# Performance work log

Measured on AMD Instinct MI355X. Metric: run time of the kernel, lower is better.

## Reference

```python
import jax, jax.numpy as jnp
import numpy as np

NUM = 8          # nlk*nlk - 1
IDX_REF = 4      # center neighbor index


def _gather2d(img, yi, xi):
    # img: (B,H,W); yi,xi: int32 (B,K,H,W) already clipped in-range
    B, H, W = img.shape
    flat = img.reshape(B, H * W)
    idx = (yi * W + xi).reshape(B, -1)
    return jnp.take_along_axis(flat, idx, axis=1).reshape(yi.shape)


def _bilinear(img, ys, xs):
    # bilinear sample with zero padding outside (deform-conv v2 semantics)
    # img: (B,H,W); ys,xs: float (B,K,H,W)
    B, H, W = img.shape
    y0 = jnp.floor(ys)
    x0 = jnp.floor(xs)
    y0i = y0.astype(jnp.int32)
    x0i = x0.astype(jnp.int32)
    wy1 = ys - y0
    wx1 = xs - x0
    out = jnp.zeros(ys.shape, img.dtype)
    for dy, wy in ((0, 1.0 - wy1), (1, wy1)):
        for dx, wx in ((0, 1.0 - wx1), (1, wx1)):
            yy = y0i + dy
            xx = x0i + dx
            valid = ((yy >= 0) & (yy < H) & (xx >= 0) & (xx < W)).astype(img.dtype)
            v = _gather2d(img, jnp.clip(yy, 0, H - 1), jnp.clip(xx, 0, W - 1))
            out = out + wy * wx * valid * v
    return out


def _conv3(x, w):
    return jax.lax.conv_general_dilated(x, w, (1, 1), ((1, 1), (1, 1)),
                                        dimension_numbers=('NCHW', 'OIHW', 'NCHW'))


def _bn_relu(x, g, b, m, v):
    s = g / jnp.sqrt(v + 1e-5)
    return jax.nn.relu(x * s[None, :, None, None] + (b - m * s)[None, :, None, None])


def _disp_warp(right, disp):
    # sample right image at x' = x - disparity, bilinear along width, zeros outside
    B, C, H, W = right.shape
    xs = jnp.arange(W, dtype=right.dtype)[None, None, :] - disp[:, 0]  # (B,H,W)
    x0 = jnp.floor(xs)
    x0i = x0.astype(jnp.int32)
    w1 = xs - x0
    out = jnp.zeros_like(right)
    for d, w in ((0, 1.0 - w1), (1, w1)):
        xi = x0i + d
        valid = ((xi >= 0) & (xi < W)).astype(right.dtype)
        v = jnp.take_along_axis(right, jnp.clip(xi, 0, W - 1)[:, None], axis=3)
        out = out + (w * valid)[:, None] * v
    return out


def _forward(coarse_disparity, normal_estimation, left_image, right_image, confidence,
             conv1_w, bn1_g, bn1_b, bn1_m, bn1_v,
             conv2_w, bn2_g, bn2_b, bn2_m, bn2_v,
             conv3_w, aff_scale_const):
    B, _, H, W = coarse_disparity.shape
    # current_scale == 1 => interpolate is identity, disp_ == coarse_disparity
    warped_error = _disp_warp(right_image, coarse_disparity) - left_image
    guidance = jnp.concatenate([normal_estimation, left_image, right_image, warped_error], axis=1)

    x = _bn_relu(_conv3(guidance, conv1_w), bn1_g, bn1_b, bn1_m, bn1_v)
    x = _bn_relu(_conv3(x, conv2_w), bn2_g, bn2_b, bn2_m, bn2_v)
    oa = _conv3(x, conv3_w)                                   # (B, 3*NUM, H, W)

    o1, o2, aff = oa[:, :NUM], oa[:, NUM:2 * NUM], oa[:, 2 * NUM:]
    # torch: cat((o1,o2),1).view(B,NUM,2,H,W) -> faithful pairing of channels
    off = jnp.concatenate([o1, o2], axis=1).reshape(B, NUM, 2, H, W)
    zero_c = jnp.zeros((B, 1, 2, H, W), off.dtype)
    off9 = jnp.concatenate([off[:, :IDX_REF], zero_c, off[:, IDX_REF:]], axis=1)  # (B,9,2,H,W)

    aff = jnp.tanh(aff) / (aff_scale_const + 1e-8)            # TGASS

    # confidence gather at p + offset_k (1x1 deform conv, w_conf=1), offsets detached
    ii = jnp.arange(H, dtype=off.dtype)[None, None, :, None]
    jj = jnp.arange(W, dtype=off.dtype)[None, None, None, :]
    off_nc = jax.lax.stop_gradient(
        jnp.concatenate([off9[:, :IDX_REF], off9[:, IDX_REF + 1:]], axis=1))  # (B,8,2,H,W)
    conf_aff = _bilinear(confidence[:, 0], ii + off_nc[:, :, 0], jj + off_nc[:, :, 1])
    aff = aff * conf_aff

    s = jnp.sum(jnp.abs(aff), axis=1, keepdims=True) + 1e-4
    s = jnp.maximum(s, 1.0)                                   # TGASS clamp
    aff = aff / s
    aff_ref = 1.0 - jnp.sum(aff, axis=1, keepdims=True)
    aff9 = jnp.concatenate([aff[:, :IDX_REF], aff_ref, aff[:, IDX_REF:]], axis=1)  # (B,9,H,W)

    # one propagation: modulated deformable 3x3 conv, all-ones weight, zero bias
    ky = (jnp.arange(9, dtype=off.dtype) // 3 - 1.0)[None, :, None, None]
    kx = (jnp.arange(9, dtype=off.dtype) % 3 - 1.0)[None, :, None, None]
    sampled = _bilinear(coarse_disparity[:, 0], ii + ky + off9[:, :, 0], jj + kx + off9[:, :, 1])
    inter = jnp.sum(aff9 * sampled, axis=1, keepdims=True)    # (B,1,H,W)
    inter = inter * (inter >= 0).astype(inter.dtype)
    inter = jnp.maximum(inter, 0.0)
    final = jnp.maximum(0.7 * coarse_disparity + 0.3 * inter, 0.0)
    return final


def setup_inputs() -> dict:
    key = jax.random.key(0)
    ks = jax.random.split(key, 20)
    B, H, W = 4, 384, 1280
    inp = {}
    inp['coarse_disparity'] = jax.random.uniform(ks[0], (B, 1, H, W), jnp.float32) * 40.0
    inp['normal_estimation'] = jax.random.normal(ks[1], (B, 3, H, W), jnp.float32)
    inp['left_image'] = jax.random.uniform(ks[2], (B, 3, H, W), jnp.float32)
    inp['right_image'] = jax.random.uniform(ks[3], (B, 3, H, W), jnp.float32)
    inp['confidence'] = jax.random.uniform(ks[4], (B, 1, H, W), jnp.float32)
    inp['conv1_w'] = jax.random.normal(ks[5], (32, 12, 3, 3), jnp.float32) * 0.05
    inp['bn1_g'] = jax.random.uniform(ks[6], (32,), jnp.float32) + 0.5
    inp['bn1_b'] = jax.random.normal(ks[7], (32,), jnp.float32) * 0.1
    inp['bn1_m'] = jax.random.normal(ks[8], (32,), jnp.float32) * 0.1
    inp['bn1_v'] = jax.random.uniform(ks[9], (32,), jnp.float32) + 0.5
    inp['conv2_w'] = jax.random.normal(ks[10], (64, 32, 3, 3), jnp.float32) * 0.05
    inp['bn2_g'] = jax.random.uniform(ks[11], (64,), jnp.float32) + 0.5
    inp['bn2_b'] = jax.random.normal(ks[12], (64,), jnp.float32) * 0.1
    inp['bn2_m'] = jax.random.normal(ks[13], (64,), jnp.float32) * 0.1
    inp['bn2_v'] = jax.random.uniform(ks[14], (64,), jnp.float32) + 0.5
    inp['conv3_w'] = jax.random.normal(ks[15], (3 * NUM, 64, 3, 3), jnp.float32) * 0.05
    inp['aff_scale_const'] = jnp.array([1.0 * NUM], jnp.float32)  # affinity_gamma * num
    return inp


def reference(coarse_disparity, normal_estimation, left_image, right_image, confidence,
              conv1_w, bn1_g, bn1_b, bn1_m, bn1_v,
              conv2_w, bn2_g, bn2_b, bn2_m, bn2_v,
              conv3_w, aff_scale_const):
    return _forward(coarse_disparity, normal_estimation, left_image, right_image, confidence,
                    conv1_w, bn1_g, bn1_b, bn1_m, bn1_v,
                    conv2_w, bn2_g, bn2_b, bn2_m, bn2_v,
                    conv3_w, aff_scale_const)
```

## Files before the change

kernel.cpp:

```cpp
#include <hip/hip_runtime.h>
#include <math.h>

static constexpr int B_ = 4;
static constexpr int H_ = 384;
static constexpr int W_ = 1280;
static constexpr int HW_ = H_ * W_;

typedef _Float16 f16x8 __attribute__((ext_vector_type(8)));
typedef float f32x4 __attribute__((ext_vector_type(4)));


template <int C_IN, int C_OUT>
__global__ __launch_bounds__(256) void prep_w(const float* __restrict__ w,
                                              unsigned short* __restrict__ wb)
{
  constexpr int CICH = C_IN / 32;
  constexpr int NCOT = (C_OUT + 15) / 16;
  constexpr int NE = NCOT * CICH * 9 * 512;
  int i = blockIdx.x * 256 + threadIdx.x;
  if (i >= NE) return;
  int k   = i & 31;
  int row = (i >> 5) & 15;
  int ts  = i >> 9;
  int s   = ts % 9;
  int tc  = ts / 9;
  int c   = tc % CICH;
  int t   = tc / CICH;
  int co  = t * 16 + row;
  int ci  = c * 32 + k;
  float v = 0.f;
  if (co < C_OUT) v = w[((size_t)co * C_IN + ci) * 9 + s];
  union { _Float16 f; unsigned short u; } ch;
  ch.f = (_Float16)v;
  wb[i] = ch.u;
}

__global__ __launch_bounds__(256) void prep_w1(const float* __restrict__ w,
                                               unsigned short* __restrict__ wb)
{
  constexpr int NE = 2 * 6 * 512;
  int i = blockIdx.x * 256 + threadIdx.x;
  if (i >= NE) return;
  int k    = i & 31;
  int row  = (i >> 5) & 15;
  int ts   = i >> 9;
  int chunk = ts % 6;
  int tc   = ts / 6;
  int ky   = chunk >> 1;
  int kc   = chunk & 1;
  int kx, ci;
  bool valid;
  if (kc == 0) { kx = k >> 4;  ci = k & 15; valid = (ci < 12); }
  else         { kx = 2;       ci = k & 15; valid = (k < 16) && (ci < 12); }
  int co = tc * 16 + row;
  float v = valid ? w[((size_t)co * 12 + ci) * 9 + ky * 3 + kx] : 0.f;
  union { _Float16 f; unsigned short u; } ch;
  ch.f = (_Float16)v;
  wb[i] = ch.u;
}

__global__ __launch_bounds__(256, 4) void conv1_mfma(
    const float* __restrict__ disp, const float* __restrict__ normal,
    const float* __restrict__ left, const float* __restrict__ right,
    const unsigned short* __restrict__ wb,
    const float* __restrict__ bn_g, const float* __restrict__ bn_b,
    const float* __restrict__ bn_m, const float* __restrict__ bn_v,
    unsigned short* __restrict__ out,
    int b0, int out_y0, int out_rows)
{
  constexpr int NCOT = 2;
  constexpr int TY  = 8;
  constexpr int HR  = 10;
  constexpr int TXI = 36;

  __shared__ unsigned short smem[HR * TXI * 16];

  const int tilesX = W_ / 32;
  int bb = blockIdx.x;
  const int txi = bb % tilesX; bb /= tilesX;
  const int tilesY = (out_rows + TY - 1) / TY;
  const int tyi = bb % tilesY;
  const int gi  = bb / tilesY;
  const int b   = b0 + gi;
  const int x0  = txi * 32;
  const int oy0 = out_y0 + tyi * TY;

  const int tid    = threadIdx.x;
  const int w      = tid >> 6;
  const int lane15 = tid & 15;
  const int kgrp   = (tid >> 4) & 3;
  const int aoff   = lane15 * 32 + kgrp * 8;

  f32x4 acc[NCOT][2][2];
#pragma unroll
  for (int i = 0; i < NCOT; i++)
#pragma unroll
    for (int rr = 0; rr < 2; rr++) {
      acc[i][rr][0] = (f32x4){0.f, 0.f, 0.f, 0.f};
      acc[i][rr][1] = (f32x4){0.f, 0.f, 0.f, 0.f};
    }

  for (int it = tid; it < HR * TXI; it += 256) {
    int row = it / TXI;
    int px  = it - row * TXI;
    int gy  = oy0 - 1 + row;
    int gx  = x0 - 2 + px;
    union { _Float16 f[16]; uint4 u[2]; } R;
    R.u[0] = (uint4){0, 0, 0, 0};
    R.u[1] = (uint4){0, 0, 0, 0};
    if (((unsigned)gy < (unsigned)H_) & ((unsigned)gx < (unsigned)W_)) {
      size_t p = (size_t)gy * W_ + gx;
      float d = disp[(size_t)b * HW_ + p];
      float xs = (float)gx - d;
      float x0f = floorf(xs);
      int xi0 = (int)x0f;
      float w1 = xs - x0f;
      int xi1 = xi0 + 1;
      float v0 = (xi0 >= 0 && xi0 < W_) ? 1.f : 0.f;
      float v1 = (xi1 >= 0 && xi1 < W_) ? 1.f : 0.f;
      int xc0 = min(max(xi0, 0), W_ - 1);
      int xc1 = min(max(xi1, 0), W_ - 1);
      float w0f = (1.f - w1) * v0;
      float w1f = w1 * v1;
#pragma unroll
      for (int c = 0; c < 3; c++) {
        const float* rrow = right + (size_t)(b * 3 + c) * HW_ + (size_t)gy * W_;
        float l = left[(size_t)(b * 3 + c) * HW_ + p];
        float n = normal[(size_t)(b * 3 + c) * HW_ + p];
        float r = rrow[gx];
        float warped = w0f * rrow[xc0] + w1f * rrow[xc1];
        R.f[c]     = (_Float16)n;
        R.f[3 + c] = (_Float16)l;
        R.f[6 + c] = (_Float16)r;
        R.f[9 + c] = (_Float16)(warped - l);
      }
    }
    unsigned short* dst = &smem[it * 16];
    *(uint4*)(dst)     = R.u[0];
    *(uint4*)(dst + 8) = R.u[1];
  }
  __syncthreads();

  f16x8 ah[NCOT];
#pragma unroll
  for (int tc = 0; tc < NCOT; tc++)
    ah[tc] = *(const f16x8*)(wb + ((size_t)(tc * 6 + 0) * 512 + aoff));
#pragma unroll
  for (int c = 0; c < 6; c++) {
    const int ky = c >> 1, kc = c & 1;
    f16x8 ahn[NCOT];
    if (c < 5) {
#pragma unroll
      for (int tc = 0; tc < NCOT; tc++)
        ahn[tc] = *(const f16x8*)(wb + ((size_t)(tc * 6 + c + 1) * 512 + aoff));
    }
#pragma unroll
    for (int rr = 0; rr < 2; rr++) {
      const int col = (kc ? 3 : 1) + lane15;
      const int e0 = ((2 * w + rr + ky) * TXI + col) * 16 + kgrp * 8;
      f16x8 b0 = *(const f16x8*)&smem[e0];
      f16x8 b1 = *(const f16x8*)&smem[e0 + 256];
#pragma unroll
      for (int tc = 0; tc < NCOT; tc++) {
        acc[tc][rr][0] = __builtin_amdgcn_mfma_f32_16x16x32_f16(
            ah[tc], b0, acc[tc][rr][0], 0, 0, 0);
        acc[tc][rr][1] = __builtin_amdgcn_mfma_f32_16x16x32_f16(
            ah[tc], b1, acc[tc][rr][1], 0, 0, 0);
      }
    }
    if (c < 5) {
#pragma unroll
      for (int tc = 0; tc < NCOT; tc++) ah[tc] = ahn[tc];
    }
  }

#pragma unroll
  for (int rr = 0; rr < 2; rr++) {
    const int orow = oy0 + 2 * w + rr;
    if (orow < out_y0 + out_rows) {
      const int ox = x0 + lane15;
#pragma unroll
      for (int tc = 0; tc < NCOT; tc++) {
        const int o = tc * 2 + (kgrp >> 1);
        const size_t recbase =
            (((size_t)(gi * 4 + o) * out_rows + (orow - out_y0)) * W_ + ox) * 8
            + (kgrp & 1) * 4;
#pragma unroll
        for (int nt = 0; nt < 2; nt++) {
          union { _Float16 f[4]; uint2 u; } Hh;
#pragma unroll
          for (int j = 0; j < 4; j++) {
            const int co = tc * 16 + kgrp * 4 + j;
            float s = bn_g[co] * rsqrtf(bn_v[co] + 1e-5f);
            float v = fmaxf(acc[tc][rr][nt][j] * s + (bn_b[co] - bn_m[co] * s), 0.f);
            Hh.f[j] = (_Float16)v;
          }
          *(uint2*)&out[recbase + (size_t)nt * 128] = Hh.u;
        }
      }
    }
  }
}

template <int C_IN, int C_OUT, bool BNRELU, int OUTMODE, int MINW>
__global__ __launch_bounds__(256, MINW) void conv3x3_mfma(
    const unsigned short* __restrict__ in, const unsigned short* __restrict__ wb,
    const float* __restrict__ bn_g, const float* __restrict__ bn_b,
    const float* __restrict__ bn_m, const float* __restrict__ bn_v,
    void* __restrict__ out,
    int in_y0, int in_rows, int out_y0, int out_rows)
{
  constexpr int CICH = C_IN / 32;
  constexpr int NCIO = C_IN / 8;
  constexpr int NCOT = (C_OUT + 15) / 16;
  constexpr int TY  = 8;
  constexpr int HR  = 10;
  constexpr int TXI = 36;
  constexpr int PX2 = 18;
  constexpr int PXW = 36;

  __shared__ unsigned short smem[HR * TXI * PXW];

  const int tilesX = W_ / 32;
  int bb = blockIdx.x;
  const int txi = bb % tilesX; bb /= tilesX;
  const int tilesY = (out_rows + TY - 1) / TY;
  const int tyi = bb % tilesY;
  const int gi  = bb / tilesY;
  const int x0  = txi * 32;
  const int oy0 = out_y0 + tyi * TY;

  const int tid    = threadIdx.x;
  const int w      = tid >> 6;
  const int lane15 = tid & 15;
  const int kgrp   = (tid >> 4) & 3;
  const int aoff   = lane15 * 32 + kgrp * 8;

  f32x4 acc[NCOT][2][2];
#pragma unroll
  for (int i = 0; i < NCOT; i++)
#pragma unroll
    for (int rr = 0; rr < 2; rr++) {
      acc[i][rr][0] = (f32x4){0.f, 0.f, 0.f, 0.f};
      acc[i][rr][1] = (f32x4){0.f, 0.f, 0.f, 0.f};
    }

  for (int cc = 0; cc < CICH; ++cc) {
    if (cc) __syncthreads();
    for (int it = tid; it < 4 * HR * PX2; it += 256) {
      int cib = it / (HR * PX2);
      int pos = it - cib * (HR * PX2);
      int row = pos / PX2;
      int p2  = pos - row * PX2;
      int gy  = oy0 - 1 + row;
      int by  = gy - in_y0;
      int gx  = x0 - 2 + 2 * p2;
      const bool rok = (unsigned)by < (unsigned)in_rows;
      uint4 h0 = {0,0,0,0}, h1 = {0,0,0,0};
      const unsigned short* src =
          in + (((size_t)(gi * NCIO + cc * 4 + cib) * in_rows + by) * W_ + gx) * 8;
      if (rok & ((unsigned)gx < (unsigned)W_))       h0 = *(const uint4*)(src);
      if (rok & ((unsigned)(gx + 1) < (unsigned)W_)) h1 = *(const uint4*)(src + 8);
      int base = (row * TXI + 2 * p2) * PXW + cib * 8;
      *(uint4*)&smem[base]       = h0;
      *(uint4*)&smem[base + PXW] = h1;
    }
    __syncthreads();

    f16x8 ah[NCOT];
#pragma unroll
    for (int tc = 0; tc < NCOT; tc++)
      ah[tc] = *(const f16x8*)(
          wb + ((size_t)((tc * CICH + cc) * 9 + 0) * 512 + aoff));
#pragma unroll
    for (int s = 0; s < 9; s++) {
      const int ky = s / 3, kx = s - 3 * ky;
      f16x8 ahn[NCOT];
      if (s < 8) {
#pragma unroll
        for (int tc = 0; tc < NCOT; tc++)
          ahn[tc] = *(const f16x8*)(
              wb + ((size_t)((tc * CICH + cc) * 9 + s + 1) * 512 + aoff));
      }
#pragma unroll
      for (int rr = 0; rr < 2; rr++) {
        const int e0 = ((2 * w + rr + ky) * TXI + 1 + lane15 + kx) * PXW + kgrp * 8;
        f16x8 b0 = *(const f16x8*)&smem[e0];
        f16x8 b1 = *(const f16x8*)&smem[e0 + 16 * PXW];
#pragma unroll
        for (int tc = 0; tc < NCOT; tc++) {
          acc[tc][rr][0] = __builtin_amdgcn_mfma_f32_16x16x32_f16(
              ah[tc], b0, acc[tc][rr][0], 0, 0, 0);
          acc[tc][rr][1] = __builtin_amdgcn_mfma_f32_16x16x32_f16(
              ah[tc], b1, acc[tc][rr][1], 0, 0, 0);
        }
      }
      if (s < 8) {
#pragma unroll
        for (int tc = 0; tc < NCOT; tc++) ah[tc] = ahn[tc];
      }
    }
  }

#pragma unroll
  for (int rr = 0; rr < 2; rr++) {
    const int orow = oy0 + 2 * w + rr;
    if (orow < out_y0 + out_rows) {
      const int ox = x0 + lane15;
      if constexpr (OUTMODE == 1) {
        unsigned short* outs = (unsigned short*)out;
#pragma unroll
        for (int tc = 0; tc < NCOT; tc++) {
          const int o = tc * 2 + (kgrp >> 1);
          const size_t recbase =
              (((size_t)(gi * (C_OUT / 8) + o) * out_rows + (orow - out_y0)) * W_ + ox) * 8
              + (kgrp & 1) * 4;
#pragma unroll
          for (int nt = 0; nt < 2; nt++) {
            union { _Float16 f[4]; uint2 u; } Hh;
#pragma unroll
            for (int j = 0; j < 4; j++) {
              float v = acc[tc][rr][nt][j];
              if constexpr (BNRELU) {
                const int co = tc * 16 + kgrp * 4 + j;
                float s = bn_g[co] * rsqrtf(bn_v[co] + 1e-5f);
                v = fmaxf(v * s + (bn_b[co] - bn_m[co] * s), 0.f);
              }
              Hh.f[j] = (_Float16)v;
            }
            *(uint2*)&outs[recbase + (size_t)nt * 128] = Hh.u;
          }
        }
      } else if constexpr (OUTMODE == 2) {
        unsigned short* outs = (unsigned short*)out;
#pragma unroll
        for (int tc = 0; tc < NCOT; tc++) {
#pragma unroll
          for (int j = 0; j < 4; j++) {
            const int co = tc * 16 + kgrp * 4 + j;
            if (co < C_OUT) {
              float r0 = acc[tc][rr][0][j];
              float r1 = acc[tc][rr][1][j];
              if constexpr (BNRELU) {
                float sc = bn_g[co] * rsqrtf(bn_v[co] + 1e-5f);
                float of = bn_b[co] - bn_m[co] * sc;
                r0 = fmaxf(r0 * sc + of, 0.f);
                r1 = fmaxf(r1 * sc + of, 0.f);
              }
              unsigned short* bp = outs + ((size_t)(gi * C_OUT + co) * out_rows +
                                           (orow - out_y0)) * (size_t)W_;
              union { _Float16 f; unsigned short u; } c0, c1;
              c0.f = (_Float16)r0; c1.f = (_Float16)r1;
              bp[ox]      = c0.u;
              bp[ox + 16] = c1.u;
            }
          }
        }
      } else {
        float* outf = (float*)out;
#pragma unroll
        for (int tc = 0; tc < NCOT; tc++) {
#pragma unroll
          for (int j = 0; j < 4; j++) {
            const int co = tc * 16 + kgrp * 4 + j;
            if (co < C_OUT) {
              float r0 = acc[tc][rr][0][j];
              float r1 = acc[tc][rr][1][j];
              if constexpr (BNRELU) {
                float sc = bn_g[co] * rsqrtf(bn_v[co] + 1e-5f);
                float of = bn_b[co] - bn_m[co] * sc;
                r0 = fmaxf(r0 * sc + of, 0.f);
                r1 = fmaxf(r1 * sc + of, 0.f);
              }
              float* bp = outf + ((size_t)(gi * C_OUT + co) * out_rows +
                                  (orow - out_y0)) * (size_t)W_;
              bp[ox]      = r0;
              bp[ox + 16] = r1;
            }
          }
        }
      }
    }
  }
}

__device__ __forceinline__ float bilin1(const float* __restrict__ img,
                                        float ys, float xs)
{
  float y0f = floorf(ys), x0f = floorf(xs);
  int y0 = (int)y0f, x0 = (int)x0f;
  float wy1 = ys - y0f, wx1 = xs - x0f;
  float wy0 = 1.f - wy1, wx0 = 1.f - wx1;
  int y1 = y0 + 1, x1 = x0 + 1;
  float vy0 = (y0 >= 0 && y0 < H_) ? 1.f : 0.f;
  float vy1 = (y1 >= 0 && y1 < H_) ? 1.f : 0.f;
  float vx0 = (x0 >= 0 && x0 < W_) ? 1.f : 0.f;
  float vx1 = (x1 >= 0 && x1 < W_) ? 1.f : 0.f;
  int yc0 = min(max(y0, 0), H_ - 1), yc1 = min(max(y1, 0), H_ - 1);
  int xc0 = min(max(x0, 0), W_ - 1), xc1 = min(max(x1, 0), W_ - 1);
  const float* r0 = img + (size_t)yc0 * W_;
  const float* r1 = img + (size_t)yc1 * W_;
  float v00 = r0[xc0], v01 = r0[xc1], v10 = r1[xc0], v11 = r1[xc1];
  return (wy0 * vy0) * ((wx0 * vx0) * v00 + (wx1 * vx1) * v01) +
         (wy1 * vy1) * ((wx0 * vx0) * v10 + (wx1 * vx1) * v11);
}

__global__ __launch_bounds__(256) void final_band(
    const unsigned short* __restrict__ oa, const float* __restrict__ conf,
    const float* __restrict__ disp, const float* __restrict__ asc,
    float* __restrict__ out, int b0, int g, int y0g, int rows)
{
  int idx = blockIdx.x * 256 + threadIdx.x;
  if (idx >= g * rows * W_) return;
  int x = idx % W_;
  int t = idx / W_;
  int yr = t % rows;
  int gi = t / rows;
  int y = y0g + yr;
  int b = b0 + gi;
  int p = y * W_ + x;

  const float scale = 1.f / (asc[0] + 1e-8f);
  const float* cimg = conf + (size_t)b * HW_;
  const float* dimg = disp + (size_t)b * HW_;
  const unsigned short* oab = oa + (size_t)gi * 24 * rows * W_;
  const size_t cs = (size_t)rows * W_;
  const size_t q = (size_t)yr * W_ + x;

  float offy[8], offx[8], a[8];
#pragma unroll
  for (int k = 0; k < 8; k++) {
    offy[k] = (float)(*(const _Float16*)&oab[(size_t)k * cs + q]);
    offx[k] = (float)(*(const _Float16*)&oab[(size_t)(8 + k) * cs + q]);
    float ar = (float)(*(const _Float16*)&oab[(size_t)(16 + k) * cs + q]);
    float ca = bilin1(cimg, (float)y + offy[k], (float)x + offx[k]);
    a[k] = tanhf(ar) * scale * ca;
  }

  float s = 1e-4f;
#pragma unroll
  for (int k = 0; k < 8; k++) s += fabsf(a[k]);
  s = fmaxf(s, 1.f);
  float inv = 1.f / s;
  float suma = 0.f;
#pragma unroll
  for (int k = 0; k < 8; k++) { a[k] *= inv; suma += a[k]; }
  float aref = 1.f - suma;

  float inter = 0.f;
#pragma unroll
  for (int k9 = 0; k9 < 9; k9++) {
    float oy, ox, w;
    if (k9 < 4)       { oy = offy[k9];     ox = offx[k9];     w = a[k9]; }
    else if (k9 == 4) { oy = 0.f;          ox = 0.f;          w = aref;  }
    else              { oy = offy[k9 - 1]; ox = offx[k9 - 1]; w = a[k9 - 1]; }
    float ky = (float)(k9 / 3) - 1.f;
    float kx = (float)(k9 % 3) - 1.f;
    inter += w * bilin1(dimg, (float)y + ky + oy, (float)x + kx + ox);
  }
  inter = fmaxf(inter, 0.f);
  float cd = dimg[p];
  out[(size_t)b * HW_ + p] = fmaxf(0.7f * cd + 0.3f * inter, 0.f);
}

extern "C" void kernel_launch(void* const* d_in, const int* in_sizes, int n_in,
                              void* d_out, int out_size, void* d_ws, size_t ws_size,
                              hipStream_t stream)
{
  const float* disp   = (const float*)d_in[0];
  const float* normal = (const float*)d_in[1];
  const float* left   = (const float*)d_in[2];
  const float* right  = (const float*)d_in[3];
  const float* conf   = (const float*)d_in[4];
  const float* w1     = (const float*)d_in[5];
  const float* g1     = (const float*)d_in[6];
  const float* b1     = (const float*)d_in[7];
  const float* m1     = (const float*)d_in[8];
  const float* v1     = (const float*)d_in[9];
  const float* w2     = (const float*)d_in[10];
  const float* g2     = (const float*)d_in[11];
  const float* b2     = (const float*)d_in[12];
  const float* m2     = (const float*)d_in[13];
  const float* v2     = (const float*)d_in[14];
  const float* w3     = (const float*)d_in[15];
  const float* asc    = (const float*)d_in[16];
  float* out = (float*)d_out;

  constexpr int WB1E = 2 * 6 * 512;
  constexpr int WB2E = 4 * 1 * 9 * 512;
  constexpr int WB3E = 2 * 2 * 9 * 512;
  const size_t wbytes = (size_t)(WB1E + WB2E + WB3E) * sizeof(unsigned short);

  struct Cfg { int g, bh; };
  const Cfg cfgs[] = {{4, 384}, {2, 384}, {1, 384}, {4, 96}, {2, 96},
                      {1, 96}, {1, 48}, {1, 24}, {1, 12}, {1, 8}, {1, 4}};
  int G = 1, BH = 4;
  for (const Cfg& c : cfgs) {
    size_t bytes = (size_t)c.g * W_ *
                   (64u * (c.bh + 4) + 128u * (c.bh + 2));
    if (bytes + wbytes <= ws_size) { G = c.g; BH = c.bh; break; }
  }

  unsigned short* x1s = (unsigned short*)d_ws;
  unsigned short* x2s = x1s + (size_t)G * 32 * (BH + 4) * W_;
  unsigned short* oa_buf = (unsigned short*)d_ws;
  unsigned short* wb1 = x2s + (size_t)G * 64 * (BH + 2) * W_;
  unsigned short* wb2 = wb1 + WB1E;
  unsigned short* wb3 = wb2 + WB2E;

  prep_w1<<<(WB1E + 255) / 256, 256, 0, stream>>>(w1, wb1);
  prep_w<32, 64><<<(WB2E + 255) / 256, 256, 0, stream>>>(w2, wb2);
  prep_w<64, 24><<<(WB3E + 255) / 256, 256, 0, stream>>>(w3, wb3);

  const int tilesX = W_ / 32;

  for (int b0 = 0; b0 < B_; b0 += G) {
    for (int y0 = 0; y0 < H_; y0 += BH) {
      const int rows_out = min(BH, H_ - y0);
      const int y_x2_0 = max(y0 - 1, 0);
      const int y_x2_1 = min(y0 + rows_out + 1, H_);
      const int rows_x2 = y_x2_1 - y_x2_0;
      const int y_x1_0 = max(y0 - 2, 0);
      const int y_x1_1 = min(y0 + rows_out + 2, H_);
      const int rows_x1 = y_x1_1 - y_x1_0;

      {
        int grid = tilesX * ((rows_x1 + 7) / 8) * G;
        conv1_mfma<<<grid, 256, 0, stream>>>(
            disp, normal, left, right, wb1, g1, b1, m1, v1, x1s,
            b0, y_x1_0, rows_x1);
      }
      {
        int grid = tilesX * ((rows_x2 + 7) / 8) * G;
        conv3x3_mfma<32, 64, true, 1, 4><<<grid, 256, 0, stream>>>(
            x1s, wb2, g2, b2, m2, v2, (void*)x2s,
            y_x1_0, rows_x1, y_x2_0, rows_x2);
      }
      {
        int grid = tilesX * ((rows_out + 7) / 8) * G;
        conv3x3_mfma<64, 24, false, 2, 4><<<grid, 256, 0, stream>>>(
            x2s, wb3, nullptr, nullptr, nullptr, nullptr, (void*)oa_buf,
            y_x2_0, rows_x2, y0, rows_out);
      }
      {
        int n = G * rows_out * W_;
        final_band<<<(n + 255) / 256, 256, 0, stream>>>(
            oa_buf, conf, disp, asc, out, b0, G, y0, rows_out);
      }
    }
  }
}
```

Measured before the change: 575.4 us.

## Fuse conv3 with final affinity propagation via shared-memory staging

Measured after the change: 560.7 us. 1.03x faster.

```diff
diff --git a/kernel.cpp b/kernel.cpp
--- a/kernel.cpp
+++ b/kernel.cpp
@@ -202,17 +202,17 @@
   }
 }
 
-template <int C_IN, int C_OUT, bool BNRELU, int OUTMODE, int MINW>
-__global__ __launch_bounds__(256, MINW) void conv3x3_mfma(
+__global__ __launch_bounds__(256, 4) void conv2_mfma(
     const unsigned short* __restrict__ in, const unsigned short* __restrict__ wb,
     const float* __restrict__ bn_g, const float* __restrict__ bn_b,
     const float* __restrict__ bn_m, const float* __restrict__ bn_v,
-    void* __restrict__ out,
+    unsigned short* __restrict__ out,
     int in_y0, int in_rows, int out_y0, int out_rows)
 {
-  constexpr int CICH = C_IN / 32;
-  constexpr int NCIO = C_IN / 8;
-  constexpr int NCOT = (C_OUT + 15) / 16;
+  constexpr int C_IN = 32, C_OUT = 64;
+  constexpr int CICH = 1;
+  constexpr int NCIO = 4;
+  constexpr int NCOT = 4;
   constexpr int TY  = 8;
   constexpr int HR  = 10;
   constexpr int TXI = 36;
@@ -227,6 +227,151 @@
   const int tilesY = (out_rows + TY - 1) / TY;
   const int tyi = bb % tilesY;
   const int gi  = bb / tilesY;
+  const int x0  = txi * 32;
+  const int oy0 = out_y0 + tyi * TY;
+
+  const int tid    = threadIdx.x;
+  const int w      = tid >> 6;
+  const int lane15 = tid & 15;
+  const int kgrp   = (tid >> 4) & 3;
+  const int aoff   = lane15 * 32 + kgrp * 8;
+
+  f32x4 acc[NCOT][2][2];
+#pragma unroll
+  for (int i = 0; i < NCOT; i++)
+#pragma unroll
+    for (int rr = 0; rr < 2; rr++) {
+      acc[i][rr][0] = (f32x4){0.f, 0.f, 0.f, 0.f};
+      acc[i][rr][1] = (f32x4){0.f, 0.f, 0.f, 0.f};
+    }
+
+  for (int it = tid; it < 4 * HR * PX2; it += 256) {
+    int cib = it / (HR * PX2);
+    int pos = it - cib * (HR * PX2);
+    int row = pos / PX2;
+    int p2  = pos - row * PX2;
+    int gy  = oy0 - 1 + row;
+    int by  = gy - in_y0;
+    int gx  = x0 - 2 + 2 * p2;
+    const bool rok = (unsigned)by < (unsigned)in_rows;
+    uint4 h0 = {0,0,0,0}, h1 = {0,0,0,0};
+    const unsigned short* src =
+        in + (((size_t)(gi * NCIO + cib) * in_rows + by) * W_ + gx) * 8;
+    if (rok & ((unsigned)gx < (unsigned)W_))       h0 = *(const uint4*)(src);
+    if (rok & ((unsigned)(gx + 1) < (unsigned)W_)) h1 = *(const uint4*)(src + 8);
+    int base = (row * TXI + 2 * p2) * PXW + cib * 8;
+    *(uint4*)&smem[base]       = h0;
+    *(uint4*)&smem[base + PXW] = h1;
+  }
+  __syncthreads();
+
+  f16x8 ah[NCOT];
+#pragma unroll
+  for (int tc = 0; tc < NCOT; tc++)
+    ah[tc] = *(const f16x8*)(wb + ((size_t)(tc * 9) * 512 + aoff));
+#pragma unroll
+  for (int s = 0; s < 9; s++) {
+    const int ky = s / 3, kx = s - 3 * ky;
+    f16x8 ahn[NCOT];
+    if (s < 8) {
+#pragma unroll
+      for (int tc = 0; tc < NCOT; tc++)
+        ahn[tc] = *(const f16x8*)(wb + ((size_t)(tc * 9 + s + 1) * 512 + aoff));
+    }
+#pragma unroll
+    for (int rr = 0; rr < 2; rr++) {
+      const int e0 = ((2 * w + rr + ky) * TXI + 1 + lane15 + kx) * PXW + kgrp * 8;
+      f16x8 b0 = *(const f16x8*)&smem[e0];
+      f16x8 b1 = *(const f16x8*)&smem[e0 + 16 * PXW];
+#pragma unroll
+      for (int tc = 0; tc < NCOT; tc++) {
+        acc[tc][rr][0] = __builtin_amdgcn_mfma_f32_16x16x32_f16(
+            ah[tc], b0, acc[tc][rr][0], 0, 0, 0);
+        acc[tc][rr][1] = __builtin_amdgcn_mfma_f32_16x16x32_f16(
+            ah[tc], b1, acc[tc][rr][1], 0, 0, 0);
+      }
+    }
+    if (s < 8) {
+#pragma unroll
+      for (int tc = 0; tc < NCOT; tc++) ah[tc] = ahn[tc];
+    }
+  }
+
+#pragma unroll
+  for (int rr = 0; rr < 2; rr++) {
+    const int orow = oy0 + 2 * w + rr;
+    if (orow < out_y0 + out_rows) {
+      const int ox = x0 + lane15;
+#pragma unroll
+      for (int tc = 0; tc < NCOT; tc++) {
+        const int o = tc * 2 + (kgrp >> 1);
+        const size_t recbase =
+            (((size_t)(gi * 8 + o) * out_rows + (orow - out_y0)) * W_ + ox) * 8
+            + (kgrp & 1) * 4;
+#pragma unroll
+        for (int nt = 0; nt < 2; nt++) {
+          union { _Float16 f[4]; uint2 u; } Hh;
+#pragma unroll
+          for (int j = 0; j < 4; j++) {
+            const int co = tc * 16 + kgrp * 4 + j;
+            float s = bn_g[co] * rsqrtf(bn_v[co] + 1e-5f);
+            float v = fmaxf(acc[tc][rr][nt][j] * s + (bn_b[co] - bn_m[co] * s), 0.f);
+            Hh.f[j] = (_Float16)v;
+          }
+          *(uint2*)&out[recbase + (size_t)nt * 128] = Hh.u;
+        }
+      }
+    }
+  }
+}
+
+__device__ __forceinline__ float bilin1(const float* __restrict__ img,
+                                        float ys, float xs)
+{
+  float y0f = floorf(ys), x0f = floorf(xs);
+  int y0 = (int)y0f, x0 = (int)x0f;
+  float wy1 = ys - y0f, wx1 = xs - x0f;
+  float wy0 = 1.f - wy1, wx0 = 1.f - wx1;
+  int y1 = y0 + 1, x1 = x0 + 1;
+  float vy0 = (y0 >= 0 && y0 < H_) ? 1.f : 0.f;
+  float vy1 = (y1 >= 0 && y1 < H_) ? 1.f : 0.f;
+  float vx0 = (x0 >= 0 && x0 < W_) ? 1.f : 0.f;
+  float vx1 = (x1 >= 0 && x1 < W_) ? 1.f : 0.f;
+  int yc0 = min(max(y0, 0), H_ - 1), yc1 = min(max(y1, 0), H_ - 1);
+  int xc0 = min(max(x0, 0), W_ - 1), xc1 = min(max(x1, 0), W_ - 1);
+  const float* r0 = img + (size_t)yc0 * W_;
+  const float* r1 = img + (size_t)yc1 * W_;
+  float v00 = r0[xc0], v01 = r0[xc1], v10 = r1[xc0], v11 = r1[xc1];
+  return (wy0 * vy0) * ((wx0 * vx0) * v00 + (wx1 * vx1) * v01) +
+         (wy1 * vy1) * ((wx0 * vx0) * v10 + (wx1 * vx1) * v11);
+}
+
+__global__ __launch_bounds__(256, 4) void conv3_final(
+    const unsigned short* __restrict__ in, const unsigned short* __restrict__ wb,
+    const float* __restrict__ conf, const float* __restrict__ disp,
+    const float* __restrict__ asc, float* __restrict__ outp,
+    int b0, int in_y0, int in_rows, int out_y0, int out_rows)
+{
+  constexpr int NCIO = 8;
+  constexpr int CICH = 2;
+  constexpr int NCOT = 2;
+  constexpr int TY  = 8;
+  constexpr int HR  = 10;
+  constexpr int TXI = 36;
+  constexpr int PX2 = 18;
+  constexpr int PXW = 36;
+  constexpr int COS = 260;
+
+  __shared__ unsigned short smem[HR * TXI * PXW];
+  float* oal = (float*)smem;
+
+  const int tilesX = W_ / 32;
+  int bb = blockIdx.x;
+  const int txi = bb % tilesX; bb /= tilesX;
+  const int tilesY = (out_rows + TY - 1) / TY;
+  const int tyi = bb % tilesY;
+  const int gi  = bb / tilesY;
+  const int b   = b0 + gi;
   const int x0  = txi * 32;
   const int oy0 = out_y0 + tyi * TY;
 
@@ -271,7 +416,7 @@
 #pragma unroll
     for (int tc = 0; tc < NCOT; tc++)
       ah[tc] = *(const f16x8*)(
-          wb + ((size_t)((tc * CICH + cc) * 9 + 0) * 512 + aoff));
+          wb + ((size_t)((tc * CICH + cc) * 9) * 512 + aoff));
 #pragma unroll
     for (int s = 0; s < 9; s++) {
       const int ky = s / 3, kx = s - 3 * ky;
@@ -302,165 +447,71 @@
     }
   }
 
-#pragma unroll
-  for (int rr = 0; rr < 2; rr++) {
-    const int orow = oy0 + 2 * w + rr;
-    if (orow < out_y0 + out_rows) {
-      const int ox = x0 + lane15;
-      if constexpr (OUTMODE == 1) {
-        unsigned short* outs = (unsigned short*)out;
-#pragma unroll
-        for (int tc = 0; tc < NCOT; tc++) {
-          const int o = tc * 2 + (kgrp >> 1);
-          const size_t recbase =
-              (((size_t)(gi * (C_OUT / 8) + o) * out_rows + (orow - out_y0)) * W_ + ox) * 8
-              + (kgrp & 1) * 4;
-#pragma unroll
-          for (int nt = 0; nt < 2; nt++) {
-            union { _Float16 f[4]; uint2 u; } Hh;
-#pragma unroll
-            for (int j = 0; j < 4; j++) {
-              float v = acc[tc][rr][nt][j];
-              if constexpr (BNRELU) {
-                const int co = tc * 16 + kgrp * 4 + j;
-                float s = bn_g[co] * rsqrtf(bn_v[co] + 1e-5f);
-                v = fmaxf(v * s + (bn_b[co] - bn_m[co] * s), 0.f);
-              }
-              Hh.f[j] = (_Float16)v;
-            }
-            *(uint2*)&outs[recbase + (size_t)nt * 128] = Hh.u;
-          }
+  __syncthreads();
+#pragma unroll
+  for (int tc = 0; tc < NCOT; tc++) {
+#pragma unroll
+    for (int j = 0; j < 4; j++) {
+      const int co = tc * 16 + kgrp * 4 + j;
+      if (co < 24) {
+#pragma unroll
+        for (int rr = 0; rr < 2; rr++) {
+          const int row = 2 * w + rr;
+#pragma unroll
+          for (int nt = 0; nt < 2; nt++)
+            oal[co * COS + row * 32 + lane15 + nt * 16] = acc[tc][rr][nt][j];
         }
-      } else if constexpr (OUTMODE == 2) {
-        unsigned short* outs = (unsigned short*)out;
-#pragma unroll
-        for (int tc = 0; tc < NCOT; tc++) {
-#pragma unroll
-          for (int j = 0; j < 4; j++) {
-            const int co = tc * 16 + kgrp * 4 + j;
-            if (co < C_OUT) {
-              float r0 = acc[tc][rr][0][j];
-              float r1 = acc[tc][rr][1][j];
-              if constexpr (BNRELU) {
-                float sc = bn_g[co] * rsqrtf(bn_v[co] + 1e-5f);
-                float of = bn_b[co] - bn_m[co] * sc;
-                r0 = fmaxf(r0 * sc + of, 0.f);
-                r1 = fmaxf(r1 * sc + of, 0.f);
-              }
-              unsigned short* bp = outs + ((size_t)(gi * C_OUT + co) * out_rows +
-                                           (orow - out_y0)) * (size_t)W_;
-              union { _Float16 f; unsigned short u; } c0, c1;
-              c0.f = (_Float16)r0; c1.f = (_Float16)r1;
-              bp[ox]      = c0.u;
-              bp[ox + 16] = c1.u;
-            }
-          }
-        }
-      } else {
-        float* outf = (float*)out;
-#pragma unroll
-        for (int tc = 0; tc < NCOT; tc++) {
-#pragma unroll
-          for (int j = 0; j < 4; j++) {
-            const int co = tc * 16 + kgrp * 4 + j;
-            if (co < C_OUT) {
-              float r0 = acc[tc][rr][0][j];
-              float r1 = acc[tc][rr][1][j];
-              if constexpr (BNRELU) {
-                float sc = bn_g[co] * rsqrtf(bn_v[co] + 1e-5f);
-                float of = bn_b[co] - bn_m[co] * sc;
-                r0 = fmaxf(r0 * sc + of, 0.f);
-                r1 = fmaxf(r1 * sc + of, 0.f);
-              }
-              float* bp = outf + ((size_t)(gi * C_OUT + co) * out_rows +
-                                  (orow - out_y0)) * (size_t)W_;
-              bp[ox]      = r0;
-              bp[ox + 16] = r1;
-            }
-          }
-        }
-      }
-    }
-  }
-}
-
-__device__ __forceinline__ float bilin1(const float* __restrict__ img,
-                                        float ys, float xs)
-{
-  float y0f = floorf(ys), x0f = floorf(xs);
-  int y0 = (int)y0f, x0 = (int)x0f;
-  float wy1 = ys - y0f, wx1 = xs - x0f;
-  float wy0 = 1.f - wy1, wx0 = 1.f - wx1;
-  int y1 = y0 + 1, x1 = x0 + 1;
-  float vy0 = (y0 >= 0 && y0 < H_) ? 1.f : 0.f;
-  float vy1 = (y1 >= 0 && y1 < H_) ? 1.f : 0.f;
-  float vx0 = (x0 >= 0 && x0 < W_) ? 1.f : 0.f;
-  float vx1 = (x1 >= 0 && x1 < W_) ? 1.f : 0.f;
-  int yc0 = min(max(y0, 0), H_ - 1), yc1 = min(max(y1, 0), H_ - 1);
-  int xc0 = min(max(x0, 0), W_ - 1), xc1 = min(max(x1, 0), W_ - 1);
-  const float* r0 = img + (size_t)yc0 * W_;
-  const float* r1 = img + (size_t)yc1 * W_;
-  float v00 = r0[xc0], v01 = r0[xc1], v10 = r1[xc0], v11 = r1[xc1];
-  return (wy0 * vy0) * ((wx0 * vx0) * v00 + (wx1 * vx1) * v01) +
-         (wy1 * vy1) * ((wx0 * vx0) * v10 + (wx1 * vx1) * v11);
-}
-
-__global__ __launch_bounds__(256) void final_band(
-    const unsigned short* __restrict__ oa, const float* __restrict__ conf,
-    const float* __restrict__ disp, const float* __restrict__ asc,
-    float* __restrict__ out, int b0, int g, int y0g, int rows)
-{
-  int idx = blockIdx.x * 256 + threadIdx.x;
-  if (idx >= g * rows * W_) return;
-  int x = idx % W_;
-  int t = idx / W_;
-  int yr = t % rows;
-  int gi = t / rows;
-  int y = y0g + yr;
-  int b = b0 + gi;
-  int p = y * W_ + x;
-
-  const float scale = 1.f / (asc[0] + 1e-8f);
-  const float* cimg = conf + (size_t)b * HW_;
-  const float* dimg = disp + (size_t)b * HW_;
-  const unsigned short* oab = oa + (size_t)gi * 24 * rows * W_;
-  const size_t cs = (size_t)rows * W_;
-  const size_t q = (size_t)yr * W_ + x;
-
-  float offy[8], offx[8], a[8];
-#pragma unroll
-  for (int k = 0; k < 8; k++) {
-    offy[k] = (float)(*(const _Float16*)&oab[(size_t)k * cs + q]);
-    offx[k] = (float)(*(const _Float16*)&oab[(size_t)(8 + k) * cs + q]);
-    float ar = (float)(*(const _Float16*)&oab[(size_t)(16 + k) * cs + q]);
-    float ca = bilin1(cimg, (float)y + offy[k], (float)x + offx[k]);
-    a[k] = tanhf(ar) * scale * ca;
-  }
-
-  float s = 1e-4f;
-#pragma unroll
-  for (int k = 0; k < 8; k++) s += fabsf(a[k]);
-  s = fmaxf(s, 1.f);
-  float inv = 1.f / s;
-  float suma = 0.f;
-#pragma unroll
-  for (int k = 0; k < 8; k++) { a[k] *= inv; suma += a[k]; }
-  float aref = 1.f - suma;
-
-  float inter = 0.f;
-#pragma unroll
-  for (int k9 = 0; k9 < 9; k9++) {
-    float oy, ox, w;
-    if (k9 < 4)       { oy = offy[k9];     ox = offx[k9];     w = a[k9]; }
-    else if (k9 == 4) { oy = 0.f;          ox = 0.f;          w = aref;  }
-    else              { oy = offy[k9 - 1]; ox = offx[k9 - 1]; w = a[k9 - 1]; }
-    float ky = (float)(k9 / 3) - 1.f;
-    float kx = (float)(k9 % 3) - 1.f;
-    inter += w * bilin1(dimg, (float)y + ky + oy, (float)x + kx + ox);
-  }
-  inter = fmaxf(inter, 0.f);
-  float cd = dimg[p];
-  out[(size_t)b * HW_ + p] = fmaxf(0.7f * cd + 0.3f * inter, 0.f);
+      }
+    }
+  }
+  __syncthreads();
+
+  const int px = tid & 31;
+  const int r  = tid >> 5;
+  const int orow = oy0 + r;
+  const int gx = x0 + px;
+  if (orow < out_y0 + out_rows) {
+    const float scale = 1.f / (asc[0] + 1e-8f);
+    const float* cimg = conf + (size_t)b * HW_;
+    const float* dimg = disp + (size_t)b * HW_;
+    const int base = r * 32 + px;
+
+    float offy[8], offx[8], a[8];
+#pragma unroll
+    for (int k = 0; k < 8; k++) {
+      offy[k] = oal[(size_t)k * COS + base];
+      offx[k] = oal[(size_t)(8 + k) * COS + base];
+      float ar = oal[(size_t)(16 + k) * COS + base];
+      float ca = bilin1(cimg, (float)orow + offy[k], (float)gx + offx[k]);
+      a[k] = tanhf(ar) * scale * ca;
+    }
+
+    float s = 1e-4f;
+#pragma unroll
+    for (int k = 0; k < 8; k++) s += fabsf(a[k]);
+    s = fmaxf(s, 1.f);
+    float inv = 1.f / s;
+    float suma = 0.f;
+#pragma unroll
+    for (int k = 0; k < 8; k++) { a[k] *= inv; suma += a[k]; }
+    float aref = 1.f - suma;
+
+    float inter = 0.f;
+#pragma unroll
+    for (int k9 = 0; k9 < 9; k9++) {
+      float oy, ox, wk;
+      if (k9 < 4)       { oy = offy[k9];     ox = offx[k9];     wk = a[k9]; }
+      else if (k9 == 4) { oy = 0.f;          ox = 0.f;          wk = aref;  }
+      else              { oy = offy[k9 - 1]; ox = offx[k9 - 1]; wk = a[k9 - 1]; }
+      float ky = (float)(k9 / 3) - 1.f;
+      float kx = (float)(k9 % 3) - 1.f;
+      inter += wk * bilin1(dimg, (float)orow + ky + oy, (float)gx + kx + ox);
+    }
+    inter = fmaxf(inter, 0.f);
+    float cd = dimg[(size_t)orow * W_ + gx];
+    outp[(size_t)b * HW_ + (size_t)orow * W_ + gx] =
+        fmaxf(0.7f * cd + 0.3f * inter, 0.f);
+  }
 }
 
 extern "C" void kernel_launch(void* const* d_in, const int* in_sizes, int n_in,
@@ -503,7 +554,6 @@
 
   unsigned short* x1s = (unsigned short*)d_ws;
   unsigned short* x2s = x1s + (size_t)G * 32 * (BH + 4) * W_;
-  unsigned short* oa_buf = (unsigned short*)d_ws;
   unsigned short* wb1 = x2s + (size_t)G * 64 * (BH + 2) * W_;
   unsigned short* wb2 = wb1 + WB1E;
   unsigned short* wb3 = wb2 + WB2E;
@@ -532,21 +582,16 @@
       }
       {
         int grid = tilesX * ((rows_x2 + 7) / 8) * G;
-        conv3x3_mfma<32, 64, true, 1, 4><<<grid, 256, 0, stream>>>(
-            x1s, wb2, g2, b2, m2, v2, (void*)x2s,
+        conv2_mfma<<<grid, 256, 0, stream>>>(
+            x1s, wb2, g2, b2, m2, v2, x2s,
             y_x1_0, rows_x1, y_x2_0, rows_x2);
       }
       {
         int grid = tilesX * ((rows_out + 7) / 8) * G;
-        conv3x3_mfma<64, 24, false, 2, 4><<<grid, 256, 0, stream>>>(
-            x2s, wb3, nullptr, nullptr, nullptr, nullptr, (void*)oa_buf,
-            y_x2_0, rows_x2, y0, rows_out);
-      }
-      {
-        int n = G * rows_out * W_;
-        final_band<<<(n + 255) / 256, 256, 0, stream>>>(
-            oa_buf, conf, disp, asc, out, b0, G, y0, rows_out);
-      }
-    }
-  }
-}
+        conv3_final<<<grid, 256, 0, stream>>>(
+            x2s, wb3, conf, disp, asc, out,
+            b0, y_x2_0, rows_x2, y0, rows_out);
+      }
+    }
+  }
+}
```
